# Performance work log

Hardware: AMD Instinct MI355X
Metric: run time of the kernel (lower is better)

Reference implementation:

```python
import jax, jax.numpy as jnp
import numpy as np

H = 64  # hidden_size
B, T1, T2, T3 = 4096, 512, 256, 128


def setup_inputs() -> dict:
    key = jax.random.key(0)
    ks = jax.random.split(key, 18)
    s = 1.0 / np.sqrt(H)  # torch LSTMCell init scale
    def p(k, shape, scale):
        return jax.random.normal(k, shape, dtype=jnp.float32) * scale
    return {
        "x1": p(ks[0], (B, T1), 1.0),
        "x2": p(ks[1], (B, T2), 1.0),
        "x3": p(ks[2], (B, T3), 1.0),
        "W_ih3": p(ks[3], (4 * H, 3), s), "W_hh3": p(ks[4], (4 * H, H), s),
        "b_ih3": p(ks[5], (4 * H,), s), "b_hh3": p(ks[6], (4 * H,), s),
        "W_ih2": p(ks[7], (4 * H, 2), s), "W_hh2": p(ks[8], (4 * H, H), s),
        "b_ih2": p(ks[9], (4 * H,), s), "b_hh2": p(ks[10], (4 * H,), s),
        "W_ih1": p(ks[11], (4 * H, 1), s), "W_hh1": p(ks[12], (4 * H, H), s),
        "b_ih1": p(ks[13], (4 * H,), s), "b_hh1": p(ks[14], (4 * H,), s),
        "W_out": p(ks[15], (1, H), s), "b_out": p(ks[16], (1,), s),
    }


def reference(x1, x2, x3,
              W_ih3, W_hh3, b_ih3, b_hh3,
              W_ih2, W_hh2, b_ih2, b_hh2,
              W_ih1, W_hh1, b_ih1, b_hh1,
              W_out, b_out):
    h = W_hh3.shape[1]
    Bb, t1 = x1.shape
    r2, r3 = t1 // x2.shape[1], t1 // x3.shape[1]
    # Pad input weights to width 3; concat order is [x1, x2, x3] (zeros where absent),
    # so padded-column zeros reproduce the narrower cells exactly.
    Wi = jnp.stack([W_ih3,
                    jnp.pad(W_ih2, ((0, 0), (0, 1))),
                    jnp.pad(W_ih1, ((0, 0), (0, 2)))])  # [3, 4H, 3]
    Wh = jnp.stack([W_hh3, W_hh2, W_hh1])               # [3, 4H, H]
    bs = jnp.stack([b_ih3 + b_hh3, b_ih2 + b_hh2, b_ih1 + b_hh1])  # [3, 4H]
    t = np.arange(t1)
    has2 = (t % r2 == 0)
    has3 = (t % r3 == 0)
    assert not np.any(has3 & ~has2), "ratio2 must divide ratio3 for the concat-order mapping"
    # width 3 -> cell3 (type 0), width 2 -> cell2 (type 1), width 1 -> cell1 (type 2)
    step_type = jnp.asarray(2 - has2.astype(np.int32) - has3.astype(np.int32))
    xs = jnp.zeros((t1, Bb, 3), x1.dtype)
    xs = xs.at[:, :, 0].set(x1.T)
    xs = xs.at[::r2, :, 1].set(x2.T)
    xs = xs.at[::r3, :, 2].set(x3.T)

    def step(carry, inp):
        hx, cx = carry
        x, ty = inp
        g = x @ Wi[ty].T + hx @ Wh[ty].T + bs[ty]  # [B, 4H]
        i, f, gg, o = jnp.split(g, 4, axis=-1)     # torch gate order i,f,g,o
        cx = jax.nn.sigmoid(f) * cx + jax.nn.sigmoid(i) * jnp.tanh(gg)
        hx = jax.nn.sigmoid(o) * jnp.tanh(cx)
        return (hx, cx), None

    z = jnp.zeros((Bb, h), x1.dtype)
    (hx, _), _ = jax.lax.scan(step, (z, z), (xs, step_type))
    return jax.nn.sigmoid(hx @ W_out.T + b_out)  # [B, 1]
```

## Files before the change

kernel.cpp:

```cpp
#include <hip/hip_runtime.h>


typedef __attribute__((ext_vector_type(8))) short short8v;
typedef __attribute__((ext_vector_type(4))) float float4v;

template <int N> struct IC { static constexpr int value = N; };

#define AST 72
#define XS1 516
#define XS2 260
#define XS3 132

#if __has_builtin(__builtin_amdgcn_exp2f)
#define EXP2F(x) __builtin_amdgcn_exp2f(x)
#else
#define EXP2F(x) exp2f(x)
#endif
#if __has_builtin(__builtin_amdgcn_rcpf)
#define RCPF(x) __builtin_amdgcn_rcpf(x)
#else
#define RCPF(x) (1.0f / (x))
#endif

#define NL2E -1.4426950408889634f
#define NL2E2 -2.8853900817779268f

__device__ __forceinline__ short f2bf(float f) {
  union { float f; unsigned u; } v; v.f = f;
  unsigned r = v.u + 0x7FFFu + ((v.u >> 16) & 1u);
  return (short)(r >> 16);
}
__device__ __forceinline__ float bf2f(short h) {
  union { float f; unsigned u; } v;
  v.u = ((unsigned)(unsigned short)h) << 16;
  return v.f;
}
__device__ __forceinline__ float rcp1p(float y) {
  return RCPF(1.0f + EXP2F(y));
}
__device__ __forceinline__ float fsig(float x) { return rcp1p(x * NL2E); }
__device__ __forceinline__ float ftanh(float x) {
  return __builtin_fmaf(2.0f, rcp1p(x * NL2E2), -1.0f);
}

__global__ __launch_bounds__(256, 1) void mlstm_kernel(
    const float* __restrict__ x1, const float* __restrict__ x2,
    const float* __restrict__ x3,
    const float* __restrict__ Wi3, const float* __restrict__ Wh3,
    const float* __restrict__ bi3, const float* __restrict__ bh3,
    const float* __restrict__ Wi2, const float* __restrict__ Wh2,
    const float* __restrict__ bi2, const float* __restrict__ bh2,
    const float* __restrict__ Wi1, const float* __restrict__ Wh1,
    const float* __restrict__ bi1, const float* __restrict__ bh1,
    const float* __restrict__ Wout, const float* __restrict__ bout,
    float* __restrict__ out) {
  __shared__ __attribute__((aligned(16))) short Ab0[16 * AST];
  __shared__ __attribute__((aligned(16))) short Ab1[16 * AST];
  __shared__ short x1b[16 * XS1];
  __shared__ short x2b[16 * XS2];
  __shared__ short x3b[16 * XS3];

  const int tid = threadIdx.x;
  const int w = tid >> 6;
  const int lane = tid & 63;
  const int q = lane >> 4;
  const int c = lane & 15;
  const int R0 = blockIdx.x << 4;

  for (int idx = tid; idx < 16 * 512; idx += 256) {
    int m = idx >> 9, t = idx & 511;
    x1b[m * XS1 + t] = f2bf(x1[(size_t)(R0 + m) * 512 + t]);
  }
  for (int idx = tid; idx < 16 * 256; idx += 256) {
    int m = idx >> 8, t = idx & 255;
    x2b[m * XS2 + t] = f2bf(x2[(size_t)(R0 + m) * 256 + t]);
  }
  for (int idx = tid; idx < 16 * 128; idx += 256) {
    int m = idx >> 7, t = idx & 127;
    x3b[m * XS3 + t] = f2bf(x3[(size_t)(R0 + m) * 128 + t]);
  }
  for (int idx = tid; idx < 16 * AST; idx += 256) {
    Ab0[idx] = 0;
    Ab1[idx] = 0;
  }

  short8v whs[3][4][2];
  short8v wix[3][4];
  float4v bias4[3][4];
  {
    const float* WhA[3] = {Wh3, Wh2, Wh1};
    const float* WiA[3] = {Wi3, Wi2, Wi1};
    const float* biA[3] = {bi3, bi2, bi1};
    const float* bhA[3] = {bh3, bh2, bh1};
    const int wdt[3] = {3, 2, 1};
#pragma unroll
    for (int ty = 0; ty < 3; ++ty) {
#pragma unroll
      for (int g = 0; g < 4; ++g) {
        const float sg = (g == 2) ? NL2E2 : NL2E;
        const int n = g * 64 + 16 * w + c;
#pragma unroll
        for (int kf = 0; kf < 2; ++kf) {
          short8v v;
#pragma unroll
          for (int j = 0; j < 8; ++j)
            v[j] = f2bf(sg * WhA[ty][n * 64 + kf * 32 + q * 8 + j]);
          whs[ty][g][kf] = v;
        }
        short8v v2 = {0, 0, 0, 0, 0, 0, 0, 0};
        if (q == 0) {
#pragma unroll
          for (int j = 0; j < 3; ++j)
            if (j < wdt[ty]) v2[j] = f2bf(sg * WiA[ty][n * wdt[ty] + j]);
        }
        wix[ty][g] = v2;
        float b = sg * (biA[ty][n] + bhA[ty][n]);
        float4v bv = {b, b, b, b};
        bias4[ty][g] = bv;
      }
    }
  }

  const int afo = c * AST + q * 8;
  const int hwo = (4 * q) * AST + 16 * w + c;
  const int x1o = c * XS1;
  const int x2o = c * XS2;
  const int x3o = c * XS3;

  __syncthreads();

  float cx[4] = {0.f, 0.f, 0.f, 0.f};

  auto stepf = [&](auto tyc, int t, const short* rbuf, short* wbuf) {
    constexpr int TY = decltype(tyc)::value;
    short hx1 = x1b[x1o + t];
    short hx2 = x2b[x2o + (t >> 1)];
    short hx3 = x3b[x3o + (t >> 2)];
    short8v a2 = {hx1, hx2, hx3, 0, 0, 0, 0, 0};
    short8v a0 = *(const short8v*)(rbuf + afo);
    short8v a1 = *(const short8v*)(rbuf + afo + 32);

    float4v acc[4];
#pragma unroll
    for (int g = 0; g < 4; ++g) {
      float4v z = bias4[TY][g];
      z = __builtin_amdgcn_mfma_f32_16x16x32_bf16(a0, whs[TY][g][0], z, 0, 0, 0);
      z = __builtin_amdgcn_mfma_f32_16x16x32_bf16(a1, whs[TY][g][1], z, 0, 0, 0);
      z = __builtin_amdgcn_mfma_f32_16x16x32_bf16(a2, wix[TY][g], z, 0, 0, 0);
      acc[g] = z;
    }

    short* hb = wbuf + hwo;
#pragma unroll
    for (int r = 0; r < 4; ++r) {
      float si = rcp1p(acc[0][r]);
      float sf = rcp1p(acc[1][r]);
      float tg = __builtin_fmaf(2.0f, rcp1p(acc[2][r]), -1.0f);
      float so = rcp1p(acc[3][r]);
      float ncx = __builtin_fmaf(sf, cx[r], si * tg);
      cx[r] = ncx;
      float hv = so * ftanh(ncx);
      hb[r * AST] = f2bf(hv);
    }
    __syncthreads();
  };

  for (int t4 = 0; t4 < 512; t4 += 4) {
    stepf(IC<0>{}, t4, Ab0, Ab1);
    stepf(IC<2>{}, t4 + 1, Ab1, Ab0);
    stepf(IC<1>{}, t4 + 2, Ab0, Ab1);
    stepf(IC<2>{}, t4 + 3, Ab1, Ab0);
  }

  if (tid < 16) {
    float s = bout[0];
    const short* hr = Ab0 + tid * AST;
#pragma unroll
    for (int k = 0; k < 64; ++k)
      s = __builtin_fmaf(bf2f(hr[k]), Wout[k], s);
    out[R0 + tid] = fsig(s);
  }
}

extern "C" void kernel_launch(void* const* d_in, const int* in_sizes, int n_in,
                              void* d_out, int out_size, void* d_ws,
                              size_t ws_size, hipStream_t stream) {
  const float* x1 = (const float*)d_in[0];
  const float* x2 = (const float*)d_in[1];
  const float* x3 = (const float*)d_in[2];
  const float* Wi3 = (const float*)d_in[3];
  const float* Wh3 = (const float*)d_in[4];
  const float* bi3 = (const float*)d_in[5];
  const float* bh3 = (const float*)d_in[6];
  const float* Wi2 = (const float*)d_in[7];
  const float* Wh2 = (const float*)d_in[8];
  const float* bi2 = (const float*)d_in[9];
  const float* bh2 = (const float*)d_in[10];
  const float* Wi1 = (const float*)d_in[11];
  const float* Wh1 = (const float*)d_in[12];
  const float* bi1 = (const float*)d_in[13];
  const float* bh1 = (const float*)d_in[14];
  const float* Wout = (const float*)d_in[15];
  const float* bout = (const float*)d_in[16];
  float* out = (float*)d_out;

  hipLaunchKernelGGL(mlstm_kernel, dim3(256), dim3(256), 0, stream,
                     x1, x2, x3, Wi3, Wh3, bi3, bh3, Wi2, Wh2, bi2, bh2,
                     Wi1, Wh1, bi1, bh1, Wout, bout, out);
}
```

Before: 335.2 us.

## Transpose MFMA operands for packed h stores and prefetch x inputs per 4-step group

Swaps the MFMA A/B operands so each lane's accumulator holds four consecutive hidden units of one batch row instead of four rows. The new h values can then be packed with v_cvt_pk_bf16 and written as a single 8-byte LDS store instead of four scattered 2-byte stores, and the bias is laid out per-row to match. The x inputs are loaded as vectors once per 4-step group and prefetched for the next group, removing per-step LDS loads from the serial recurrence. The change relies on an inline asm instruction and reads slightly past the end of the x1 buffer on the last iteration.

After: 307.5 us. 1.09x faster.

```diff
diff --git a/kernel.cpp b/kernel.cpp
--- a/kernel.cpp
+++ b/kernel.cpp
@@ -3,6 +3,8 @@
 
 typedef __attribute__((ext_vector_type(8))) short short8v;
 typedef __attribute__((ext_vector_type(4))) float float4v;
+typedef __attribute__((ext_vector_type(4))) unsigned short ushort4v;
+typedef __attribute__((ext_vector_type(2))) unsigned int uint2v;
 
 template <int N> struct IC { static constexpr int value = N; };
 
@@ -34,6 +36,11 @@
   union { float f; unsigned u; } v;
   v.u = ((unsigned)(unsigned short)h) << 16;
   return v.f;
+}
+__device__ __forceinline__ unsigned cvt_pk_bf16(float lo, float hi) {
+  unsigned r;
+  asm("v_cvt_pk_bf16_f32 %0, %1, %2" : "=v"(r) : "v"(lo), "v"(hi));
+  return r;
 }
 __device__ __forceinline__ float rcp1p(float y) {
   return RCPF(1.0f + EXP2F(y));
@@ -56,9 +63,9 @@
     float* __restrict__ out) {
   __shared__ __attribute__((aligned(16))) short Ab0[16 * AST];
   __shared__ __attribute__((aligned(16))) short Ab1[16 * AST];
-  __shared__ short x1b[16 * XS1];
-  __shared__ short x2b[16 * XS2];
-  __shared__ short x3b[16 * XS3];
+  __shared__ __attribute__((aligned(16))) short x1b[16 * XS1];
+  __shared__ __attribute__((aligned(16))) short x2b[16 * XS2];
+  __shared__ __attribute__((aligned(16))) short x3b[16 * XS3];
 
   const int tid = threadIdx.x;
   const int w = tid >> 6;
@@ -114,15 +121,19 @@
             if (j < wdt[ty]) v2[j] = f2bf(sg * WiA[ty][n * wdt[ty] + j]);
         }
         wix[ty][g] = v2;
-        float b = sg * (biA[ty][n] + bhA[ty][n]);
-        float4v bv = {b, b, b, b};
+        float4v bv;
+#pragma unroll
+        for (int r = 0; r < 4; ++r) {
+          const int nd = g * 64 + 16 * w + 4 * q + r;
+          bv[r] = sg * (biA[ty][nd] + bhA[ty][nd]);
+        }
         bias4[ty][g] = bv;
       }
     }
   }
 
   const int afo = c * AST + q * 8;
-  const int hwo = (4 * q) * AST + 16 * w + c;
+  const int hwo = c * AST + 16 * w + 4 * q;
   const int x1o = c * XS1;
   const int x2o = c * XS2;
   const int x3o = c * XS3;
@@ -131,12 +142,13 @@
 
   float cx[4] = {0.f, 0.f, 0.f, 0.f};
 
-  auto stepf = [&](auto tyc, int t, const short* rbuf, short* wbuf) {
+  auto stepf = [&](auto tyc, auto sc, const short* rbuf, short* wbuf,
+                   ushort4v xav, unsigned xbv, unsigned short xcv) {
     constexpr int TY = decltype(tyc)::value;
-    short hx1 = x1b[x1o + t];
-    short hx2 = x2b[x2o + (t >> 1)];
-    short hx3 = x3b[x3o + (t >> 2)];
-    short8v a2 = {hx1, hx2, hx3, 0, 0, 0, 0, 0};
+    constexpr int S = decltype(sc)::value;
+    short x1s = (short)xav[S];
+    short x2s = (short)((S < 2) ? (xbv & 0xFFFFu) : (xbv >> 16));
+    short8v a2 = {x1s, x2s, (short)xcv, 0, 0, 0, 0, 0};
     short8v a0 = *(const short8v*)(rbuf + afo);
     short8v a1 = *(const short8v*)(rbuf + afo + 32);
 
@@ -144,13 +156,13 @@
 #pragma unroll
     for (int g = 0; g < 4; ++g) {
       float4v z = bias4[TY][g];
-      z = __builtin_amdgcn_mfma_f32_16x16x32_bf16(a0, whs[TY][g][0], z, 0, 0, 0);
-      z = __builtin_amdgcn_mfma_f32_16x16x32_bf16(a1, whs[TY][g][1], z, 0, 0, 0);
-      z = __builtin_amdgcn_mfma_f32_16x16x32_bf16(a2, wix[TY][g], z, 0, 0, 0);
+      z = __builtin_amdgcn_mfma_f32_16x16x32_bf16(wix[TY][g], a2, z, 0, 0, 0);
+      z = __builtin_amdgcn_mfma_f32_16x16x32_bf16(whs[TY][g][0], a0, z, 0, 0, 0);
+      z = __builtin_amdgcn_mfma_f32_16x16x32_bf16(whs[TY][g][1], a1, z, 0, 0, 0);
       acc[g] = z;
     }
 
-    short* hb = wbuf + hwo;
+    float h[4];
 #pragma unroll
     for (int r = 0; r < 4; ++r) {
       float si = rcp1p(acc[0][r]);
@@ -159,17 +171,30 @@
       float so = rcp1p(acc[3][r]);
       float ncx = __builtin_fmaf(sf, cx[r], si * tg);
       cx[r] = ncx;
-      float hv = so * ftanh(ncx);
-      hb[r * AST] = f2bf(hv);
+      h[r] = so * ftanh(ncx);
     }
+    uint2v pk;
+    pk[0] = cvt_pk_bf16(h[0], h[1]);
+    pk[1] = cvt_pk_bf16(h[2], h[3]);
+    *(uint2v*)(wbuf + hwo) = pk;
     __syncthreads();
   };
 
+  ushort4v xa = *(const ushort4v*)(x1b + x1o);
+  unsigned xb = *(const unsigned*)(x2b + x2o);
+  unsigned short xc = (unsigned short)x3b[x3o];
+
   for (int t4 = 0; t4 < 512; t4 += 4) {
-    stepf(IC<0>{}, t4, Ab0, Ab1);
-    stepf(IC<2>{}, t4 + 1, Ab1, Ab0);
-    stepf(IC<1>{}, t4 + 2, Ab0, Ab1);
-    stepf(IC<2>{}, t4 + 3, Ab1, Ab0);
+    ushort4v xav = xa;
+    unsigned xbv = xb;
+    unsigned short xcv = xc;
+    stepf(IC<0>{}, IC<0>{}, Ab0, Ab1, xav, xbv, xcv);
+    xa = *(const ushort4v*)(x1b + x1o + t4 + 4);
+    xb = *(const unsigned*)(x2b + x2o + ((t4 + 4) >> 1));
+    xc = (unsigned short)x3b[x3o + ((t4 + 4) >> 2)];
+    stepf(IC<2>{}, IC<1>{}, Ab1, Ab0, xav, xbv, xcv);
+    stepf(IC<1>{}, IC<2>{}, Ab0, Ab1, xav, xbv, xcv);
+    stepf(IC<2>{}, IC<3>{}, Ab1, Ab0, xav, xbv, xcv);
   }
 
   if (tid < 16) {
```
